# Kernel tuning notes

Hardware: AMD Instinct MI355X
Metric: run time of the kernel (lower is better)

The kernel has to match this reference:

```python
import math
import jax, jax.numpy as jnp
import numpy as np

B, H, W, C = 16, 64, 64, 192
WS, SHIFT, NH = 16, 8, 6
D = C // NH
N = WS * WS
HID = 4 * C
EPS = 1e-5


def _static_tables():
    # relative position index (N, N)
    coords = np.stack(np.meshgrid(np.arange(WS), np.arange(WS), indexing='ij'))  # (2, WS, WS)
    cf = coords.reshape(2, -1)
    rel = (cf[:, :, None] - cf[:, None, :]).transpose(1, 2, 0)  # (N, N, 2)
    rel[:, :, 0] += WS - 1
    rel[:, :, 1] += WS - 1
    rel[:, :, 0] *= 2 * WS - 1
    rel_idx = rel.sum(-1)  # (N, N)
    # log-spaced continuous relative coords table ((2WS-1)^2, 2)
    r = np.arange(-(WS - 1), WS, dtype=np.float32)
    tab = np.stack(np.meshgrid(r, r, indexing='ij'), axis=-1)  # (2WS-1, 2WS-1, 2)
    tab = tab / (WS - 1) * 8.0
    tab = np.sign(tab) * np.log2(np.abs(tab) + 1.0) / np.log2(8.0)
    # shifted-window attention mask (nW, N, N)
    img = np.zeros((H, W))
    cnt = 0
    for hs in (slice(0, -WS), slice(-WS, -SHIFT), slice(-SHIFT, None)):
        for ws_ in (slice(0, -WS), slice(-WS, -SHIFT), slice(-SHIFT, None)):
            img[hs, ws_] = cnt
            cnt += 1
    win = img.reshape(H // WS, WS, W // WS, WS).transpose(0, 2, 1, 3).reshape(-1, N)
    diff = win[:, None, :] - win[:, :, None]
    mask = np.where(diff != 0, -100.0, 0.0).astype(np.float32)
    return jnp.asarray(rel_idx), jnp.asarray(tab.reshape(-1, 2)), jnp.asarray(mask)

REL_IDX, CPB_TABLE, ATTN_MASK = _static_tables()


def setup_inputs() -> dict:
    key = jax.random.key(0)
    ks = jax.random.split(key, 24)
    s = 0.02
    return {
        'hidden_states': jax.random.normal(ks[0], (B, H * W, C), jnp.float32),
        'time': jax.random.uniform(ks[1], (B,), jnp.float32),
        'q_w': jax.random.normal(ks[2], (C, C), jnp.float32) * s,
        'q_b': jnp.zeros((C,), jnp.float32),
        'k_w': jax.random.normal(ks[3], (C, C), jnp.float32) * s,
        'v_w': jax.random.normal(ks[4], (C, C), jnp.float32) * s,
        'v_b': jnp.zeros((C,), jnp.float32),
        'logit_scale': jnp.full((NH, 1, 1), math.log(10.0), jnp.float32),
        'cpb_w1': jax.random.normal(ks[5], (512, 2), jnp.float32) * s,
        'cpb_b1': jnp.zeros((512,), jnp.float32),
        'cpb_w2': jax.random.normal(ks[6], (NH, 512), jnp.float32) * s,
        'proj_w': jax.random.normal(ks[7], (C, C), jnp.float32) * s,
        'proj_b': jnp.zeros((C,), jnp.float32),
        'ln1_ww': jax.random.normal(ks[8], (C, 1), jnp.float32) * s,
        'ln1_wb': jnp.ones((C,), jnp.float32),
        'ln1_bw': jax.random.normal(ks[9], (C, 1), jnp.float32) * s,
        'ln1_bb': jnp.zeros((C,), jnp.float32),
        'fc1_w': jax.random.normal(ks[10], (HID, C), jnp.float32) * s,
        'fc1_b': jnp.zeros((HID,), jnp.float32),
        'fc2_w': jax.random.normal(ks[11], (C, HID), jnp.float32) * s,
        'fc2_b': jnp.zeros((C,), jnp.float32),
        'ln2_ww': jax.random.normal(ks[12], (C, 1), jnp.float32) * s,
        'ln2_wb': jnp.ones((C,), jnp.float32),
        'ln2_bw': jax.random.normal(ks[13], (C, 1), jnp.float32) * s,
        'ln2_bb': jnp.zeros((C,), jnp.float32),
    }


def _cond_ln(x, time, ww, wb, bw, bb):
    mean = x.mean(-1, keepdims=True)
    var = (x ** 2).mean(-1, keepdims=True) - mean ** 2
    xn = (x - mean) / jnp.sqrt(var + EPS)
    t = time.reshape(-1, 1)
    w = (t @ ww.T + wb)[:, None, :]
    b = (t @ bw.T + bb)[:, None, :]
    return w * xn + b


def _forward(hidden_states, time, q_w, q_b, k_w, v_w, v_b, logit_scale,
             cpb_w1, cpb_b1, cpb_w2, proj_w, proj_b,
             ln1_ww, ln1_wb, ln1_bw, ln1_bb,
             fc1_w, fc1_b, fc2_w, fc2_b,
             ln2_ww, ln2_wb, ln2_bw, ln2_bb):
    nWh, nWw = H // WS, W // WS
    nW = nWh * nWw
    x = hidden_states.reshape(B, H, W, C)
    x = jnp.roll(x, (-SHIFT, -SHIFT), axis=(1, 2))
    # window partition -> (B*nW, N, C)
    xw = x.reshape(B, nWh, WS, nWw, WS, C).transpose(0, 1, 3, 2, 4, 5).reshape(-1, N, C)
    q = (xw @ q_w.T + q_b).reshape(-1, N, NH, D).transpose(0, 2, 1, 3)
    k = (xw @ k_w.T).reshape(-1, N, NH, D).transpose(0, 2, 1, 3)
    v = (xw @ v_w.T + v_b).reshape(-1, N, NH, D).transpose(0, 2, 1, 3)
    # cosine attention with learned temperature
    qn = q / jnp.linalg.norm(q, axis=-1, keepdims=True)
    kn = k / jnp.linalg.norm(k, axis=-1, keepdims=True)
    scale = jnp.exp(jnp.minimum(logit_scale, math.log(100.0)))  # (NH,1,1)
    attn = jnp.einsum('whnd,whmd->whnm', qn, kn) * scale
    # continuous relative position bias
    tbl = jnp.maximum(CPB_TABLE @ cpb_w1.T + cpb_b1, 0.0) @ cpb_w2.T  # (M, NH)
    rpb = tbl[REL_IDX.reshape(-1)].reshape(N, N, NH).transpose(2, 0, 1)
    attn = attn + 16.0 * jax.nn.sigmoid(rpb)[None]
    # shifted-window mask
    attn = attn.reshape(B, nW, NH, N, N) + ATTN_MASK[None, :, None]
    attn = jax.nn.softmax(attn.reshape(-1, NH, N, N), axis=-1)
    out = jnp.einsum('whnm,whmd->whnd', attn, v).transpose(0, 2, 1, 3).reshape(-1, N, C)
    out = out @ proj_w.T + proj_b
    # window reverse + un-roll
    out = out.reshape(B, nWh, nWw, WS, WS, C).transpose(0, 1, 3, 2, 4, 5).reshape(B, H, W, C)
    out = jnp.roll(out, (SHIFT, SHIFT), axis=(1, 2)).reshape(B, H * W, C)
    # res-post-norm residual blocks
    h = hidden_states + _cond_ln(out, time, ln1_ww, ln1_wb, ln1_bw, ln1_bb)
    mlp = jax.nn.gelu(h @ fc1_w.T + fc1_b, approximate=False) @ fc2_w.T + fc2_b
    return h + _cond_ln(mlp, time, ln2_ww, ln2_wb, ln2_bw, ln2_bb)


def reference(hidden_states, time, q_w, q_b, k_w, v_w, v_b, logit_scale,
              cpb_w1, cpb_b1, cpb_w2, proj_w, proj_b,
              ln1_ww, ln1_wb, ln1_bw, ln1_bb,
              fc1_w, fc1_b, fc2_w, fc2_b,
              ln2_ww, ln2_wb, ln2_bw, ln2_bb):
    return _forward(hidden_states, time, q_w, q_b, k_w, v_w, v_b, logit_scale,
                    cpb_w1, cpb_b1, cpb_w2, proj_w, proj_b,
                    ln1_ww, ln1_wb, ln1_bw, ln1_bb,
                    fc1_w, fc1_b, fc2_w, fc2_b,
                    ln2_ww, ln2_wb, ln2_bw, ln2_bb)
```

## Files before the change

kernel.cpp:

```cpp
#include <hip/hip_runtime.h>
#include <hip/hip_bf16.h>
#include <hip/hip_fp16.h>
#include <math.h>

#define BB 16
#define CC 192
#define SHIFT 8
#define NH 6
#define DD 32
#define NN 256
#define HID 768
#define NWIN 256
#define NROWS 65536

#define OFF_TBL   0ll
#define OFF_BIASM (32ll<<10)
#define OFF_WQKV  (3200ll<<10)
#define OFF_PWB   (3424ll<<10)
#define OFF_W1B   (3500ll<<10)
#define OFF_W2B   (3800ll<<10)
#define OFF_BQKV  (4096ll<<10)
#define OFF_WTAB  (4104ll<<10)
#define OFF_XB    (8ll<<20)
#define OFF_Q     (32ll<<20)
#define OFF_K     (56ll<<20)
#define OFF_V     (80ll<<20)
#define OFF_AO    (104ll<<20)
#define OFF_HB    OFF_XB
#define OFF_H2    OFF_Q

typedef __attribute__((ext_vector_type(4)))  float f32x4;
typedef __attribute__((ext_vector_type(16))) float f32x16;
typedef __attribute__((ext_vector_type(8)))  short bf16x8;

__device__ __forceinline__ void gload16(const void* g, void* l) {
    __builtin_amdgcn_global_load_lds(
        (const __attribute__((address_space(1))) void*)g,
        (__attribute__((address_space(3))) void*)l, 16, 0, 0);
}

__device__ __forceinline__ float b2f(short s) {
    unsigned u = ((unsigned)(unsigned short)s) << 16;
    return __builtin_bit_cast(float, u);
}
__device__ __forceinline__ short f2b(float f) {
    return __builtin_bit_cast(short, __float2bfloat16(f));
}
__device__ __forceinline__ unsigned pk2(float lo, float hi) {
    unsigned a = (unsigned short)f2b(lo);
    unsigned b = (unsigned short)f2b(hi);
    return a | (b << 16);
}

__device__ __forceinline__ float fexp2(float x) {
#if __has_builtin(__builtin_amdgcn_exp2f)
    return __builtin_amdgcn_exp2f(x);
#else
    return __expf(x * 0.69314718056f);
#endif
}

__device__ __forceinline__ float gelu_fast(float x) {
    float x2 = x * x;
    float z = x * fmaf(0.0713548353f, x2, 1.5957691216f);
    float e = __expf(-z);
    return x * __builtin_amdgcn_rcpf(1.0f + e);
}

__device__ __forceinline__ float cpb_coord(int u) {
    float t = (float)u * (8.0f / 15.0f);
    return copysignf(log2f(fabsf(t) + 1.0f) * (1.0f / 3.0f), t);
}

__global__ __launch_bounds__(512) void k_tbl(
    const float* __restrict__ w1, const float* __restrict__ b1,
    const float* __restrict__ w2, float* __restrict__ tbl)
{
    __shared__ float r[512];
    int m = blockIdx.x;
    int a = m / 31, b = m % 31;
    float c0 = cpb_coord(a - 15);
    float c1 = cpb_coord(b - 15);
    int hd = threadIdx.x;
    float rv = c0 * w1[hd * 2 + 0] + c1 * w1[hd * 2 + 1] + b1[hd];
    r[hd] = fmaxf(rv, 0.0f);
    __syncthreads();
    if (hd < NH) {
        float s = 0.0f;
        for (int k = 0; k < 512; ++k) s += r[k] * w2[hd * 512 + k];
        tbl[m * NH + hd] = s;
    }
}

__global__ __launch_bounds__(256) void k_biasm(
    const float* __restrict__ tbl, const float* __restrict__ lscale,
    __half* __restrict__ biasp)
{
    int bid = blockIdx.x;
    int ty = bid / (NH * NN);
    int rem = bid % (NH * NN);
    int h = rem >> 8, i = rem & 255;
    int j = threadIdx.x;
    int yi = i >> 4, xi = i & 15, yj = j >> 4, xj = j & 15;
    int idx = (yi - yj + 15) * 31 + (xi - xj + 15);
    float v = 16.0f / (1.0f + __expf(-tbl[idx * NH + h]));
    int rhi = (ty & 2) ? ((yi < SHIFT) ? 1 : 2) : 0;
    int rwi = (ty & 1) ? ((xi < SHIFT) ? 1 : 2) : 0;
    int rhj = (ty & 2) ? ((yj < SHIFT) ? 1 : 2) : 0;
    int rwj = (ty & 1) ? ((xj < SHIFT) ? 1 : 2) : 0;
    if (rhi * 3 + rwi != rhj * 3 + rwj) v -= 100.0f;
    float scale = __expf(fminf(lscale[h], 4.6051702f));
    v = (v - 16.0f - scale) * 1.44269504f;
    int jc = j & 31;
    int r = (jc & 3) + 4 * (jc >> 3);
    int g = (jc >> 2) & 1;
    int pos = (j & ~31) + g * 16 + r;
    biasp[(((size_t)ty * NH + h) * NN + i) * NN + pos] = __float2half(v);
}

__global__ __launch_bounds__(256) void k_cvt(
    const float* __restrict__ qw, const float* __restrict__ kw,
    const float* __restrict__ vw, const float* __restrict__ pw,
    const float* __restrict__ fc1w, const float* __restrict__ fc2w,
    const float* __restrict__ q_b, const float* __restrict__ v_b,
    __hip_bfloat16* __restrict__ wqkv, __hip_bfloat16* __restrict__ pwb,
    __hip_bfloat16* __restrict__ w1b, __hip_bfloat16* __restrict__ w2b,
    float* __restrict__ bqkv)
{
    int i = blockIdx.x * 256 + threadIdx.x;
    const int S1 = 36864, S2 = 73728, S3 = 110592, S4 = 147456,
              S5 = 294912, S6 = 442368, S7 = 442944;
    if (i < S3) {
        const float* src = (i < S1) ? qw : (i < S2) ? kw : vw;
        int off = (i < S1) ? i : (i < S2) ? i - S1 : i - S2;
        wqkv[i] = __float2bfloat16(src[off]);
    } else if (i < S4) { pwb[i - S3] = __float2bfloat16(pw[i - S3]); }
    else if (i < S5)   { w1b[i - S4] = __float2bfloat16(fc1w[i - S4]); }
    else if (i < S6)   { w2b[i - S5] = __float2bfloat16(fc2w[i - S5]); }
    else if (i < S7) {
        int j = i - S6;
        bqkv[j] = (j < 192) ? q_b[j] : (j < 384) ? 0.0f : v_b[j - 384];
    }
}

__global__ __launch_bounds__(256) void k_wtab(
    const float* __restrict__ time,
    const float* __restrict__ w1w, const float* __restrict__ w1b_,
    const float* __restrict__ b1w, const float* __restrict__ b1b_,
    const float* __restrict__ w2w, const float* __restrict__ w2b_,
    const float* __restrict__ b2w, const float* __restrict__ b2b_,
    float* __restrict__ wtab)
{
    int idx = blockIdx.x * 256 + threadIdx.x;
    int t = idx / 3072, rem = idx % 3072;
    int b = rem / 192, c = rem % 192;
    float tm = time[b];
    float v;
    if (t == 0)      v = tm * w1w[c] + w1b_[c];
    else if (t == 1) v = tm * b1w[c] + b1b_[c];
    else if (t == 2) v = tm * w2w[c] + w2b_[c];
    else             v = tm * b2w[c] + b2b_[c];
    wtab[idx] = v;
}

__global__ __launch_bounds__(256) void k_gather(
    const float* __restrict__ x, __hip_bfloat16* __restrict__ xb)
{
    int idx = blockIdx.x * 256 + threadIdx.x;
    int r = idx / 48, c4 = idx % 48;
    int win = r >> 8, n = r & 255;
    int b = win >> 4, wh = (win >> 2) & 3, ww = win & 3;
    int yi = n >> 4, xi = n & 15;
    int sy = (wh * 16 + yi + SHIFT) & 63;
    int sx = (ww * 16 + xi + SHIFT) & 63;
    float4 v = *(const float4*)&x[((size_t)b * 4096 + sy * 64 + sx) * CC + c4 * 4];
    union { short h[4]; short4 s4; } u;
    u.h[0] = f2b(v.x); u.h[1] = f2b(v.y); u.h[2] = f2b(v.z); u.h[3] = f2b(v.w);
    *(short4*)&((short*)xb)[(size_t)r * CC + c4 * 4] = u.s4;
}

#define STAGE_SWZ(dstLds, srcPtr, ldK, nR)                                  \
    for (int r_ = 0; r_ < (nR); ++r_) {                                     \
        int off_ = r_ * 256 + tid;                                          \
        int row_ = off_ >> 3, cb_ = off_ & 7;                               \
        int ce_ = ((cb_ ^ (row_ & 7)) << 3);                                \
        gload16((srcPtr) + (size_t)row_ * (ldK) + ce_, &(dstLds)[off_ * 8]); \
    }

__global__ __launch_bounds__(256) void k_qkvgemm(
    const __hip_bfloat16* __restrict__ A, const __hip_bfloat16* __restrict__ Bw,
    const float* __restrict__ bias, const float* __restrict__ lscale,
    __hip_bfloat16* __restrict__ qbo, __hip_bfloat16* __restrict__ kbo,
    __hip_bfloat16* __restrict__ vbo)
{
    __shared__ short lds[12288];
    short* As = lds;
    short* Bs = lds + 8192;
    int tid = threadIdx.x, lane = tid & 63;
    int w = tid >> 6, wr = w >> 1, wc = w & 1;
    int bm = blockIdx.x, bn = blockIdx.y;

    f32x4 acc[4][2];
    #pragma unroll
    for (int fm = 0; fm < 4; ++fm)
        #pragma unroll
        for (int fn = 0; fn < 2; ++fn) acc[fm][fn] = (f32x4)0.0f;

    for (int kt = 0; kt < CC; kt += 64) {
        STAGE_SWZ(As, A + (size_t)(bm * 128) * CC + kt, CC, 4)
        STAGE_SWZ(Bs, Bw + (size_t)(bn * 64) * CC + kt, CC, 2)
        __syncthreads();
        #pragma unroll
        for (int kk = 0; kk < 2; ++kk) {
            int kcq = kk * 4 + (lane >> 4);
            bf16x8 af[4], bfr[2];
            #pragma unroll
            for (int fm = 0; fm < 4; ++fm) {
                int row = wr * 64 + fm * 16 + (lane & 15);
                af[fm] = *(const bf16x8*)&As[row * 64 + ((kcq ^ (row & 7)) << 3)];
            }
            #pragma unroll
            for (int fn = 0; fn < 2; ++fn) {
                int row = wc * 32 + fn * 16 + (lane & 15);
                bfr[fn] = *(const bf16x8*)&Bs[row * 64 + ((kcq ^ (row & 7)) << 3)];
            }
            #pragma unroll
            for (int fm = 0; fm < 4; ++fm)
                #pragma unroll
                for (int fn = 0; fn < 2; ++fn)
                    acc[fm][fn] = __builtin_amdgcn_mfma_f32_16x16x32_bf16(
                        af[fm], bfr[fn], acc[fm][fn], 0, 0, 0);
        }
        __syncthreads();
    }

    bool donorm = (bn < 6);
    bool isq = (bn < 3);
    float qscale = __expf(fminf(lscale[(bn % 3) * 2 + wc], 4.6051702f)) * 1.44269504f;
    int bcol = bn * 64 + wc * 32 + (lane & 15);
    #pragma unroll
    for (int fm = 0; fm < 4; ++fm)
        #pragma unroll
        for (int r = 0; r < 4; ++r) {
            float v0 = acc[fm][0][r] + bias[bcol];
            float v1 = acc[fm][1][r] + bias[bcol + 16];
            if (donorm) {
                float s2 = v0 * v0 + v1 * v1;
                s2 += __shfl_xor(s2, 1);
                s2 += __shfl_xor(s2, 2);
                s2 += __shfl_xor(s2, 4);
                s2 += __shfl_xor(s2, 8);
                float rn = rsqrtf(s2);
                if (isq) rn *= qscale;
                v0 *= rn; v1 *= rn;
            }
            int rowl = wr * 64 + fm * 16 + ((lane >> 4) << 2) + r;
            int c0 = wc * 32 + (lane & 15);
            int sw = (rowl & 3) << 4;
            lds[rowl * 64 + (c0 ^ sw)] = f2b(v0);
            lds[rowl * 64 + ((c0 + 16) ^ sw)] = f2b(v1);
        }
    __syncthreads();
    __hip_bfloat16* dst = (bn < 3) ? qbo : (bn < 6) ? kbo : vbo;
    int cb0 = (bn % 3) * 64;
    #pragma unroll
    for (int rr = 0; rr < 2; ++rr) {
        int row = rr * 64 + (tid >> 2);
        int cl = (tid & 3) * 16;
        int cp = cl ^ ((row & 3) << 4);
        bf16x8 a = *(const bf16x8*)&lds[row * 64 + cp];
        bf16x8 b = *(const bf16x8*)&lds[row * 64 + cp + 8];
        size_t base = (size_t)(bm * 128 + row) * CC + cb0 + cl;
        *(bf16x8*)&dst[base] = a;
        *(bf16x8*)&dst[base + 8] = b;
    }
}

#define VTP 260
__global__ __launch_bounds__(256, 3) void k_attn(
    const __hip_bfloat16* __restrict__ qb,
    const __hip_bfloat16* __restrict__ kb,
    const __hip_bfloat16* __restrict__ vb,
    const __half* __restrict__ biasp,
    __hip_bfloat16* __restrict__ ao)
{
    __shared__ short Vt[32 * VTP];
    int blk = blockIdx.x;
    int win = blk / NH, h = blk % NH;
    int wwh = (win >> 2) & 3, www = win & 3;
    int ty = (((wwh == 3) ? 2 : 0) | ((www == 3) ? 1 : 0));
    int tid = threadIdx.x;
    int wv = tid >> 6, lane = tid & 63;
    int c = lane & 31, g = lane >> 5;

    {
        int j = wv * 64 + lane;
        const short* vsrc = (const short*)vb + ((size_t)(win * NN + j)) * CC + h * DD;
        #pragma unroll
        for (int q4 = 0; q4 < 4; ++q4) {
            bf16x8 t = *(const bf16x8*)(vsrc + q4 * 8);
            #pragma unroll
            for (int e = 0; e < 8; ++e)
                Vt[(q4 * 8 + e) * VTP + j] = t[e];
        }
    }
    __syncthreads();

    const short* qsrc = (const short*)qb + ((size_t)(win * NN + wv * 64)) * CC + h * DD;
    bf16x8 qf[2][2];
    #pragma unroll
    for (int fq = 0; fq < 2; ++fq)
        #pragma unroll
        for (int kd = 0; kd < 2; ++kd)
            qf[fq][kd] = *(const bf16x8*)(qsrc + (size_t)(32 * fq + c) * CC + 16 * kd + 8 * g);

    f32x16 acc_o[2];
    acc_o[0] = (f32x16)0.0f; acc_o[1] = (f32x16)0.0f;
    float lsum[2] = {0.0f, 0.0f};

    const short* kbase = (const short*)kb + ((size_t)(win * NN)) * CC + h * DD;
    const __half* bbase = biasp + (((size_t)ty * NH + h) * NN) * NN;

    for (int t = 0; t < 4; ++t) {
        int jt = t * 64;
        #pragma unroll
        for (int fj = 0; fj < 2; ++fj) {
            int jb = jt + 32 * fj;
            bf16x8 kf0 = *(const bf16x8*)(kbase + (size_t)(jb + c) * CC + 8 * g);
            bf16x8 kf1 = *(const bf16x8*)(kbase + (size_t)(jb + c) * CC + 16 + 8 * g);
            f32x16 st[2];
            __builtin_amdgcn_s_setprio(1);
            {
                f32x16 t0 = __builtin_amdgcn_mfma_f32_32x32x16_bf16(
                    kf0, qf[0][0], (f32x16)0.0f, 0, 0, 0);
                st[0] = __builtin_amdgcn_mfma_f32_32x32x16_bf16(
                    kf1, qf[0][1], t0, 0, 0, 0);
                f32x16 t1 = __builtin_amdgcn_mfma_f32_32x32x16_bf16(
                    kf0, qf[1][0], (f32x16)0.0f, 0, 0, 0);
                st[1] = __builtin_amdgcn_mfma_f32_32x32x16_bf16(
                    kf1, qf[1][1], t1, 0, 0, 0);
            }
            __builtin_amdgcn_s_setprio(0);
            bf16x8 vfr[2];
            #pragma unroll
            for (int rb = 0; rb < 2; ++rb) {
                int j0 = jb + 16 * rb + 4 * g;
                uint2 va = *(const uint2*)&Vt[c * VTP + j0];
                uint2 vb2 = *(const uint2*)&Vt[c * VTP + j0 + 8];
                union { unsigned u[4]; bf16x8 v; } vu;
                vu.u[0] = va.x; vu.u[1] = va.y; vu.u[2] = vb2.x; vu.u[3] = vb2.y;
                vfr[rb] = vu.v;
            }
            #pragma unroll
            for (int fq = 0; fq < 2; ++fq) {
                const __half* bp = bbase + (size_t)(wv * 64 + 32 * fq + c) * NN
                                   + jb + g * 16;
                union { uint4 u; __half2 h2[4]; } ba, bbu;
                ba.u  = *(const uint4*)bp;
                bbu.u = *(const uint4*)(bp + 8);
                float p[16];
                #pragma unroll
                for (int q4 = 0; q4 < 4; ++q4) {
                    float2 fa = __half22float2(ba.h2[q4]);
                    p[2 * q4 + 0] = st[fq][2 * q4 + 0] + fa.x;
                    p[2 * q4 + 1] = st[fq][2 * q4 + 1] + fa.y;
                    float2 fb = __half22float2(bbu.h2[q4]);
                    p[8 + 2 * q4 + 0] = st[fq][8 + 2 * q4 + 0] + fb.x;
                    p[8 + 2 * q4 + 1] = st[fq][8 + 2 * q4 + 1] + fb.y;
                }
                #pragma unroll
                for (int r = 0; r < 16; ++r) p[r] = fexp2(p[r]);
                #pragma unroll
                for (int r = 0; r < 16; ++r) lsum[fq] += p[r];
                union { unsigned u[4]; bf16x8 v; } pu0, pu1;
                pu0.u[0] = pk2(p[0],  p[1]);  pu0.u[1] = pk2(p[2],  p[3]);
                pu0.u[2] = pk2(p[4],  p[5]);  pu0.u[3] = pk2(p[6],  p[7]);
                pu1.u[0] = pk2(p[8],  p[9]);  pu1.u[1] = pk2(p[10], p[11]);
                pu1.u[2] = pk2(p[12], p[13]); pu1.u[3] = pk2(p[14], p[15]);
                __builtin_amdgcn_s_setprio(1);
                acc_o[fq] = __builtin_amdgcn_mfma_f32_32x32x16_bf16(
                    pu0.v, vfr[0], acc_o[fq], 0, 0, 0);
                acc_o[fq] = __builtin_amdgcn_mfma_f32_32x32x16_bf16(
                    pu1.v, vfr[1], acc_o[fq], 0, 0, 0);
                __builtin_amdgcn_s_setprio(0);
            }
        }
    }

    #pragma unroll
    for (int fq = 0; fq < 2; ++fq) {
        lsum[fq] += __shfl_xor(lsum[fq], 32);
        float rlv = 1.0f / lsum[fq];
        #pragma unroll
        for (int r = 0; r < 16; ++r) {
            int rho = (r & 3) + 8 * (r >> 2) + 4 * g;
            float rli = __shfl(rlv, rho);
            int row = wv * 64 + 32 * fq + rho;
            ao[((size_t)(win * NN + row)) * CC + h * DD + c] =
                __float2bfloat16(acc_o[fq][r] * rli);
        }
    }
}

__global__ __launch_bounds__(256) void k_projgemm(
    const __hip_bfloat16* __restrict__ ao,
    const __hip_bfloat16* __restrict__ pwb,
    const float* __restrict__ pbias,
    const float* __restrict__ wtab,
    __hip_bfloat16* xbhb)
{
    __shared__ short lds[16384];
    __shared__ float part[64][4];
    short* As = lds;
    short* Bs = lds + 4096;
    int tid = threadIdx.x, lane = tid & 63;
    int w = tid >> 6, wr = w >> 1, wc = w & 1;
    int bm = blockIdx.x;

    f32x4 acc[2][6];
    #pragma unroll
    for (int fm = 0; fm < 2; ++fm)
        #pragma unroll
        for (int fn = 0; fn < 6; ++fn) acc[fm][fn] = (f32x4)0.0f;

    for (int kt = 0; kt < CC; kt += 64) {
        STAGE_SWZ(As, ao + (size_t)(bm * 64) * CC + kt, CC, 2)
        STAGE_SWZ(Bs, pwb + kt, CC, 6)
        __syncthreads();
        #pragma unroll
        for (int kk = 0; kk < 2; ++kk) {
            int kcq = kk * 4 + (lane >> 4);
            bf16x8 af[2], bfr[6];
            #pragma unroll
            for (int fm = 0; fm < 2; ++fm) {
                int row = wr * 32 + fm * 16 + (lane & 15);
                af[fm] = *(const bf16x8*)&As[row * 64 + ((kcq ^ (row & 7)) << 3)];
            }
            #pragma unroll
            for (int fn = 0; fn < 6; ++fn) {
                int row = wc * 96 + fn * 16 + (lane & 15);
                bfr[fn] = *(const bf16x8*)&Bs[row * 64 + ((kcq ^ (row & 7)) << 3)];
            }
            #pragma unroll
            for (int fm = 0; fm < 2; ++fm)
                #pragma unroll
                for (int fn = 0; fn < 6; ++fn)
                    acc[fm][fn] = __builtin_amdgcn_mfma_f32_16x16x32_bf16(
                        af[fm], bfr[fn], acc[fm][fn], 0, 0, 0);
        }
        __syncthreads();
    }

    #pragma unroll
    for (int fm = 0; fm < 2; ++fm)
        #pragma unroll
        for (int r = 0; r < 4; ++r) {
            int rowl = wr * 32 + fm * 16 + ((lane >> 4) << 2) + r;
            float s = 0.0f, s2 = 0.0f;
            #pragma unroll
            for (int fn = 0; fn < 6; ++fn) {
                int col = wc * 96 + fn * 16 + (lane & 15);
                float v = acc[fm][fn][r] + pbias[col];
                lds[rowl * 200 + col] = f2b(v);
                s += v; s2 += v * v;
            }
            #pragma unroll
            for (int m = 1; m < 16; m <<= 1) {
                s  += __shfl_xor(s, m);
                s2 += __shfl_xor(s2, m);
            }
            if ((lane & 15) == 0) {
                part[rowl][wc * 2]     = s;
                part[rowl][wc * 2 + 1] = s2;
            }
        }
    __syncthreads();

    int row = tid >> 2;
    int cb = (tid & 3) * 48;
    float s  = part[row][0] + part[row][2];
    float s2 = part[row][1] + part[row][3];
    float mean = s * (1.0f / 192.0f);
    float rstd = rsqrtf(s2 * (1.0f / 192.0f) - mean * mean + 1e-5f);
    int rw = bm * 64 + row;
    const float* wt = wtab + (rw >> 12) * 192;
    const float* bt = wtab + 16 * 192 + (rw >> 12) * 192;
    #pragma unroll
    for (int c8 = 0; c8 < 6; ++c8) {
        int c = cb + c8 * 8;
        bf16x8 lv = *(const bf16x8*)&lds[row * 200 + c];
        bf16x8 xv = *(const bf16x8*)&xbhb[(size_t)rw * CC + c];
        float4 w0 = *(const float4*)&wt[c], w1 = *(const float4*)&wt[c + 4];
        float4 b0 = *(const float4*)&bt[c], b1 = *(const float4*)&bt[c + 4];
        float wv[8] = {w0.x, w0.y, w0.z, w0.w, w1.x, w1.y, w1.z, w1.w};
        float bv[8] = {b0.x, b0.y, b0.z, b0.w, b1.x, b1.y, b1.z, b1.w};
        bf16x8 o;
        #pragma unroll
        for (int e = 0; e < 8; ++e) {
            float xn = (b2f(lv[e]) - mean) * rstd;
            o[e] = f2b(b2f(xv[e]) + wv[e] * xn + bv[e]);
        }
        *(bf16x8*)&xbhb[(size_t)rw * CC + c] = o;
    }
}

__global__ __launch_bounds__(256) void k_fc1(
    const __hip_bfloat16* __restrict__ A, const __hip_bfloat16* __restrict__ Bw,
    const float* __restrict__ bias, __hip_bfloat16* __restrict__ Cout)
{
    __shared__ short lds[16384];
    short* As = lds;
    short* Bs = lds + 8192;
    int tid = threadIdx.x;
    int lane = tid & 63;
    int w = tid >> 6, wr = w >> 1, wc = w & 1;
    int bm = blockIdx.x, bn = blockIdx.y;

    f32x4 acc[4][4];
    #pragma unroll
    for (int fm = 0; fm < 4; ++fm)
        #pragma unroll
        for (int fn = 0; fn < 4; ++fn)
            acc[fm][fn] = (f32x4)0.0f;

    for (int kt = 0; kt < CC; kt += 64) {
        STAGE_SWZ(As, A + (size_t)(bm * 128) * CC + kt, CC, 4)
        STAGE_SWZ(Bs, Bw + (size_t)(bn * 128) * CC + kt, CC, 4)
        __syncthreads();
        #pragma unroll
        for (int kk = 0; kk < 2; ++kk) {
            int kcq = kk * 4 + (lane >> 4);
            bf16x8 af[4], bfr[4];
            #pragma unroll
            for (int fm = 0; fm < 4; ++fm) {
                int row = wr * 64 + fm * 16 + (lane & 15);
                af[fm] = *(const bf16x8*)&As[row * 64 + ((kcq ^ (row & 7)) << 3)];
            }
            #pragma unroll
            for (int fn = 0; fn < 4; ++fn) {
                int row = wc * 64 + fn * 16 + (lane & 15);
                bfr[fn] = *(const bf16x8*)&Bs[row * 64 + ((kcq ^ (row & 7)) << 3)];
            }
            #pragma unroll
            for (int fm = 0; fm < 4; ++fm)
                #pragma unroll
                for (int fn = 0; fn < 4; ++fn)
                    acc[fm][fn] = __builtin_amdgcn_mfma_f32_16x16x32_bf16(
                        af[fm], bfr[fn], acc[fm][fn], 0, 0, 0);
        }
        __syncthreads();
    }

    #pragma unroll
    for (int fm = 0; fm < 4; ++fm)
        #pragma unroll
        for (int fn = 0; fn < 4; ++fn) {
            int coll = wc * 64 + fn * 16 + (lane & 15);
            float bv = bias[bn * 128 + coll];
            #pragma unroll
            for (int r = 0; r < 4; ++r) {
                int rowl = wr * 64 + fm * 16 + ((lane >> 4) << 2) + r;
                float v = gelu_fast(acc[fm][fn][r] + bv);
                lds[rowl * 128 + (coll ^ ((rowl & 7) << 4))] = f2b(v);
            }
        }
    __syncthreads();
    #pragma unroll
    for (int rr = 0; rr < 4; ++rr) {
        int row = rr * 32 + (tid >> 3);
        int cl = (tid & 7) * 16;
        int cp = cl ^ ((row & 7) << 4);
        bf16x8 a = *(const bf16x8*)&lds[row * 128 + cp];
        bf16x8 b = *(const bf16x8*)&lds[row * 128 + cp + 8];
        size_t base = (size_t)(bm * 128 + row) * HID + bn * 128 + cl;
        *(bf16x8*)&Cout[base] = a;
        *(bf16x8*)&Cout[base + 8] = b;
    }
}

__global__ __launch_bounds__(256) void k_fc2ln(
    const __hip_bfloat16* __restrict__ A,
    const __hip_bfloat16* __restrict__ Bw,
    const float* __restrict__ bias,
    const __hip_bfloat16* __restrict__ hb,
    const float* __restrict__ wtab,
    float* __restrict__ out)
{
    __shared__ short lds[16384];
    __shared__ float part[64][4];
    short* As = lds;
    short* Bs = lds + 4096;
    int tid = threadIdx.x, lane = tid & 63;
    int w = tid >> 6, wr = w >> 1, wc = w & 1;
    int bm = blockIdx.x;

    f32x4 acc[2][6];
    #pragma unroll
    for (int fm = 0; fm < 2; ++fm)
        #pragma unroll
        for (int fn = 0; fn < 6; ++fn) acc[fm][fn] = (f32x4)0.0f;

    for (int kt = 0; kt < HID; kt += 64) {
        STAGE_SWZ(As, A + (size_t)(bm * 64) * HID + kt, HID, 2)
        STAGE_SWZ(Bs, Bw + kt, HID, 6)
        __syncthreads();
        #pragma unroll
        for (int kk = 0; kk < 2; ++kk) {
            int kcq = kk * 4 + (lane >> 4);
            bf16x8 af[2], bfr[6];
            #pragma unroll
            for (int fm = 0; fm < 2; ++fm) {
                int row = wr * 32 + fm * 16 + (lane & 15);
                af[fm] = *(const bf16x8*)&As[row * 64 + ((kcq ^ (row & 7)) << 3)];
            }
            #pragma unroll
            for (int fn = 0; fn < 6; ++fn) {
                int row = wc * 96 + fn * 16 + (lane & 15);
                bfr[fn] = *(const bf16x8*)&Bs[row * 64 + ((kcq ^ (row & 7)) << 3)];
            }
            #pragma unroll
            for (int fm = 0; fm < 2; ++fm)
                #pragma unroll
                for (int fn = 0; fn < 6; ++fn)
                    acc[fm][fn] = __builtin_amdgcn_mfma_f32_16x16x32_bf16(
                        af[fm], bfr[fn], acc[fm][fn], 0, 0, 0);
        }
        __syncthreads();
    }

    #pragma unroll
    for (int fm = 0; fm < 2; ++fm)
        #pragma unroll
        for (int r = 0; r < 4; ++r) {
            int rowl = wr * 32 + fm * 16 + ((lane >> 4) << 2) + r;
            float s = 0.0f, s2 = 0.0f;
            #pragma unroll
            for (int fn = 0; fn < 6; ++fn) {
                int col = wc * 96 + fn * 16 + (lane & 15);
                float v = acc[fm][fn][r] + bias[col];
                lds[rowl * 200 + col] = f2b(v);
                s += v; s2 += v * v;
            }
            #pragma unroll
            for (int m = 1; m < 16; m <<= 1) {
                s  += __shfl_xor(s, m);
                s2 += __shfl_xor(s2, m);
            }
            if ((lane & 15) == 0) {
                part[rowl][wc * 2]     = s;
                part[rowl][wc * 2 + 1] = s2;
            }
        }
    __syncthreads();

    int row = tid >> 2;
    int cb = (tid & 3) * 48;
    float s  = part[row][0] + part[row][2];
    float s2 = part[row][1] + part[row][3];
    float mean = s * (1.0f / 192.0f);
    float rstd = rsqrtf(s2 * (1.0f / 192.0f) - mean * mean + 1e-5f);
    int rw = bm * 64 + row;
    int win = rw >> 8, n = rw & 255, b = rw >> 12;
    int wh = (win >> 2) & 3, wwn = win & 3;
    int y  = (wh * 16 + (n >> 4) + SHIFT) & 63;
    int xq = (wwn * 16 + (n & 15) + SHIFT) & 63;
    size_t rimg = (size_t)b * 4096 + y * 64 + xq;
    const float* wt = wtab + 2 * 16 * 192 + b * 192;
    const float* bt = wtab + 3 * 16 * 192 + b * 192;
    #pragma unroll
    for (int c8 = 0; c8 < 6; ++c8) {
        int c = cb + c8 * 8;
        bf16x8 lv = *(const bf16x8*)&lds[row * 200 + c];
        bf16x8 hv = *(const bf16x8*)&hb[(size_t)rw * CC + c];
        float4 w0 = *(const float4*)&wt[c], w1 = *(const float4*)&wt[c + 4];
        float4 b0 = *(const float4*)&bt[c], b1 = *(const float4*)&bt[c + 4];
        float wv[8] = {w0.x, w0.y, w0.z, w0.w, w1.x, w1.y, w1.z, w1.w};
        float bv[8] = {b0.x, b0.y, b0.z, b0.w, b1.x, b1.y, b1.z, b1.w};
        float4 o0, o1;
        float oo[8];
        #pragma unroll
        for (int e = 0; e < 8; ++e) {
            float xn = (b2f(lv[e]) - mean) * rstd;
            oo[e] = b2f(hv[e]) + wv[e] * xn + bv[e];
        }
        o0.x = oo[0]; o0.y = oo[1]; o0.z = oo[2]; o0.w = oo[3];
        o1.x = oo[4]; o1.y = oo[5]; o1.z = oo[6]; o1.w = oo[7];
        *(float4*)&out[rimg * CC + c] = o0;
        *(float4*)&out[rimg * CC + c + 4] = o1;
    }
}

extern "C" void kernel_launch(void* const* d_in, const int* in_sizes, int n_in,
                              void* d_out, int out_size, void* d_ws, size_t ws_size,
                              hipStream_t stream)
{
    const float* x        = (const float*)d_in[0];
    const float* time     = (const float*)d_in[1];
    const float* q_w      = (const float*)d_in[2];
    const float* q_b      = (const float*)d_in[3];
    const float* k_w      = (const float*)d_in[4];
    const float* v_w      = (const float*)d_in[5];
    const float* v_b      = (const float*)d_in[6];
    const float* lscale   = (const float*)d_in[7];
    const float* cpb_w1   = (const float*)d_in[8];
    const float* cpb_b1   = (const float*)d_in[9];
    const float* cpb_w2   = (const float*)d_in[10];
    const float* proj_w   = (const float*)d_in[11];
    const float* proj_b   = (const float*)d_in[12];
    const float* ln1_ww   = (const float*)d_in[13];
    const float* ln1_wb   = (const float*)d_in[14];
    const float* ln1_bw   = (const float*)d_in[15];
    const float* ln1_bb   = (const float*)d_in[16];
    const float* fc1_w    = (const float*)d_in[17];
    const float* fc1_b    = (const float*)d_in[18];
    const float* fc2_w    = (const float*)d_in[19];
    const float* fc2_b    = (const float*)d_in[20];
    const float* ln2_ww   = (const float*)d_in[21];
    const float* ln2_wb   = (const float*)d_in[22];
    const float* ln2_bw   = (const float*)d_in[23];
    const float* ln2_bb   = (const float*)d_in[24];

    char* ws = (char*)d_ws;
    float* tbl            = (float*)(ws + OFF_TBL);
    __half* biasp         = (__half*)(ws + OFF_BIASM);
    __hip_bfloat16* wqkv  = (__hip_bfloat16*)(ws + OFF_WQKV);
    __hip_bfloat16* pwb   = (__hip_bfloat16*)(ws + OFF_PWB);
    __hip_bfloat16* w1b   = (__hip_bfloat16*)(ws + OFF_W1B);
    __hip_bfloat16* w2b   = (__hip_bfloat16*)(ws + OFF_W2B);
    float* bqkv           = (float*)(ws + OFF_BQKV);
    float* wtab           = (float*)(ws + OFF_WTAB);
    __hip_bfloat16* xb    = (__hip_bfloat16*)(ws + OFF_XB);
    __hip_bfloat16* qb    = (__hip_bfloat16*)(ws + OFF_Q);
    __hip_bfloat16* kb    = (__hip_bfloat16*)(ws + OFF_K);
    __hip_bfloat16* vb    = (__hip_bfloat16*)(ws + OFF_V);
    __hip_bfloat16* ao    = (__hip_bfloat16*)(ws + OFF_AO);
    __hip_bfloat16* hb    = (__hip_bfloat16*)(ws + OFF_HB);
    __hip_bfloat16* h2    = (__hip_bfloat16*)(ws + OFF_H2);
    float* out            = (float*)d_out;

    k_tbl   <<<961, 512, 0, stream>>>(cpb_w1, cpb_b1, cpb_w2, tbl);
    k_biasm <<<4 * NH * NN, 256, 0, stream>>>(tbl, lscale, biasp);
    k_cvt   <<<1731, 256, 0, stream>>>(q_w, k_w, v_w, proj_w, fc1_w, fc2_w,
                                       q_b, v_b, wqkv, pwb, w1b, w2b, bqkv);
    k_wtab  <<<48, 256, 0, stream>>>(time, ln1_ww, ln1_wb, ln1_bw, ln1_bb,
                                     ln2_ww, ln2_wb, ln2_bw, ln2_bb, wtab);
    k_gather<<<12288, 256, 0, stream>>>(x, xb);
    k_qkvgemm<<<dim3(NROWS / 128, 9), 256, 0, stream>>>(xb, wqkv, bqkv, lscale, qb, kb, vb);
    k_attn  <<<NWIN * NH, 256, 0, stream>>>(qb, kb, vb, biasp, ao);
    k_projgemm<<<NROWS / 64, 256, 0, stream>>>(ao, pwb, proj_b, wtab, xb);
    k_fc1   <<<dim3(NROWS / 128, HID / 128), 256, 0, stream>>>(hb, w1b, fc1_b, h2);
    k_fc2ln <<<NROWS / 64, 256, 0, stream>>>(h2, w2b, fc2_b, hb, wtab, out);
}
```

Measured before the change: 249.6 us.

## Fuse fc1, GELU and fc2+LayerNorm into one MLP kernel; enlarge proj tile

Merges the fc1 GEMM, GELU and the fc2 GEMM with its conditional LayerNorm into a single kernel. Each 64-row block keeps its input rows in LDS and streams 64-wide hidden chunks through LDS, so the 65536x768 hidden activation is never written to or read from global memory. The residual input is also read back from LDS instead of global. Separately, the projection GEMM tile grows from 64 to 128 rows. The cost is more LDS per block, fewer blocks for the projection, and extra synchronisation inside the hidden-chunk loop.

```diff
diff --git a/kernel.cpp b/kernel.cpp
--- a/kernel.cpp
+++ b/kernel.cpp
@@ -27,7 +27,6 @@
 #define OFF_V     (80ll<<20)
 #define OFF_AO    (104ll<<20)
 #define OFF_HB    OFF_XB
-#define OFF_H2    OFF_Q
 
 typedef __attribute__((ext_vector_type(4)))  float f32x4;
 typedef __attribute__((ext_vector_type(16))) float f32x16;
@@ -409,31 +408,31 @@
     const float* __restrict__ wtab,
     __hip_bfloat16* xbhb)
 {
-    __shared__ short lds[16384];
-    __shared__ float part[64][4];
+    __shared__ short lds[25600];
+    __shared__ float part[128][4];
     short* As = lds;
-    short* Bs = lds + 4096;
+    short* Bs = lds + 8192;
     int tid = threadIdx.x, lane = tid & 63;
     int w = tid >> 6, wr = w >> 1, wc = w & 1;
     int bm = blockIdx.x;
 
-    f32x4 acc[2][6];
-    #pragma unroll
-    for (int fm = 0; fm < 2; ++fm)
+    f32x4 acc[4][6];
+    #pragma unroll
+    for (int fm = 0; fm < 4; ++fm)
         #pragma unroll
         for (int fn = 0; fn < 6; ++fn) acc[fm][fn] = (f32x4)0.0f;
 
     for (int kt = 0; kt < CC; kt += 64) {
-        STAGE_SWZ(As, ao + (size_t)(bm * 64) * CC + kt, CC, 2)
+        STAGE_SWZ(As, ao + (size_t)(bm * 128) * CC + kt, CC, 4)
         STAGE_SWZ(Bs, pwb + kt, CC, 6)
         __syncthreads();
         #pragma unroll
         for (int kk = 0; kk < 2; ++kk) {
             int kcq = kk * 4 + (lane >> 4);
-            bf16x8 af[2], bfr[6];
-            #pragma unroll
-            for (int fm = 0; fm < 2; ++fm) {
-                int row = wr * 32 + fm * 16 + (lane & 15);
+            bf16x8 af[4], bfr[6];
+            #pragma unroll
+            for (int fm = 0; fm < 4; ++fm) {
+                int row = wr * 64 + fm * 16 + (lane & 15);
                 af[fm] = *(const bf16x8*)&As[row * 64 + ((kcq ^ (row & 7)) << 3)];
             }
             #pragma unroll
@@ -442,7 +441,7 @@
                 bfr[fn] = *(const bf16x8*)&Bs[row * 64 + ((kcq ^ (row & 7)) << 3)];
             }
             #pragma unroll
-            for (int fm = 0; fm < 2; ++fm)
+            for (int fm = 0; fm < 4; ++fm)
                 #pragma unroll
                 for (int fn = 0; fn < 6; ++fn)
                     acc[fm][fn] = __builtin_amdgcn_mfma_f32_16x16x32_bf16(
@@ -452,10 +451,10 @@
     }
 
     #pragma unroll
-    for (int fm = 0; fm < 2; ++fm)
+    for (int fm = 0; fm < 4; ++fm)
         #pragma unroll
         for (int r = 0; r < 4; ++r) {
-            int rowl = wr * 32 + fm * 16 + ((lane >> 4) << 2) + r;
+            int rowl = wr * 64 + fm * 16 + ((lane >> 4) << 2) + r;
             float s = 0.0f, s2 = 0.0f;
             #pragma unroll
             for (int fn = 0; fn < 6; ++fn) {
@@ -476,17 +475,17 @@
         }
     __syncthreads();
 
-    int row = tid >> 2;
-    int cb = (tid & 3) * 48;
+    int row = tid >> 1;
+    int cb = (tid & 1) * 96;
     float s  = part[row][0] + part[row][2];
     float s2 = part[row][1] + part[row][3];
     float mean = s * (1.0f / 192.0f);
     float rstd = rsqrtf(s2 * (1.0f / 192.0f) - mean * mean + 1e-5f);
-    int rw = bm * 64 + row;
+    int rw = bm * 128 + row;
     const float* wt = wtab + (rw >> 12) * 192;
     const float* bt = wtab + 16 * 192 + (rw >> 12) * 192;
     #pragma unroll
-    for (int c8 = 0; c8 < 6; ++c8) {
+    for (int c8 = 0; c8 < 12; ++c8) {
         int c = cb + c8 * 8;
         bf16x8 lv = *(const bf16x8*)&lds[row * 200 + c];
         bf16x8 xv = *(const bf16x8*)&xbhb[(size_t)rw * CC + c];
@@ -504,106 +503,89 @@
     }
 }
 
-__global__ __launch_bounds__(256) void k_fc1(
-    const __hip_bfloat16* __restrict__ A, const __hip_bfloat16* __restrict__ Bw,
-    const float* __restrict__ bias, __hip_bfloat16* __restrict__ Cout)
-{
-    __shared__ short lds[16384];
-    short* As = lds;
-    short* Bs = lds + 8192;
-    int tid = threadIdx.x;
-    int lane = tid & 63;
-    int w = tid >> 6, wr = w >> 1, wc = w & 1;
-    int bm = blockIdx.x, bn = blockIdx.y;
-
-    f32x4 acc[4][4];
-    #pragma unroll
-    for (int fm = 0; fm < 4; ++fm)
-        #pragma unroll
-        for (int fn = 0; fn < 4; ++fn)
-            acc[fm][fn] = (f32x4)0.0f;
-
-    for (int kt = 0; kt < CC; kt += 64) {
-        STAGE_SWZ(As, A + (size_t)(bm * 128) * CC + kt, CC, 4)
-        STAGE_SWZ(Bs, Bw + (size_t)(bn * 128) * CC + kt, CC, 4)
-        __syncthreads();
-        #pragma unroll
-        for (int kk = 0; kk < 2; ++kk) {
-            int kcq = kk * 4 + (lane >> 4);
-            bf16x8 af[4], bfr[4];
-            #pragma unroll
-            for (int fm = 0; fm < 4; ++fm) {
-                int row = wr * 64 + fm * 16 + (lane & 15);
-                af[fm] = *(const bf16x8*)&As[row * 64 + ((kcq ^ (row & 7)) << 3)];
-            }
-            #pragma unroll
-            for (int fn = 0; fn < 4; ++fn) {
-                int row = wc * 64 + fn * 16 + (lane & 15);
-                bfr[fn] = *(const bf16x8*)&Bs[row * 64 + ((kcq ^ (row & 7)) << 3)];
-            }
-            #pragma unroll
-            for (int fm = 0; fm < 4; ++fm)
-                #pragma unroll
-                for (int fn = 0; fn < 4; ++fn)
-                    acc[fm][fn] = __builtin_amdgcn_mfma_f32_16x16x32_bf16(
-                        af[fm], bfr[fn], acc[fm][fn], 0, 0, 0);
-        }
-        __syncthreads();
-    }
-
-    #pragma unroll
-    for (int fm = 0; fm < 4; ++fm)
-        #pragma unroll
-        for (int fn = 0; fn < 4; ++fn) {
-            int coll = wc * 64 + fn * 16 + (lane & 15);
-            float bv = bias[bn * 128 + coll];
-            #pragma unroll
-            for (int r = 0; r < 4; ++r) {
-                int rowl = wr * 64 + fm * 16 + ((lane >> 4) << 2) + r;
-                float v = gelu_fast(acc[fm][fn][r] + bv);
-                lds[rowl * 128 + (coll ^ ((rowl & 7) << 4))] = f2b(v);
-            }
-        }
-    __syncthreads();
-    #pragma unroll
-    for (int rr = 0; rr < 4; ++rr) {
-        int row = rr * 32 + (tid >> 3);
-        int cl = (tid & 7) * 16;
-        int cp = cl ^ ((row & 7) << 4);
-        bf16x8 a = *(const bf16x8*)&lds[row * 128 + cp];
-        bf16x8 b = *(const bf16x8*)&lds[row * 128 + cp + 8];
-        size_t base = (size_t)(bm * 128 + row) * HID + bn * 128 + cl;
-        *(bf16x8*)&Cout[base] = a;
-        *(bf16x8*)&Cout[base + 8] = b;
-    }
-}
-
-__global__ __launch_bounds__(256) void k_fc2ln(
-    const __hip_bfloat16* __restrict__ A,
-    const __hip_bfloat16* __restrict__ Bw,
-    const float* __restrict__ bias,
+__global__ __launch_bounds__(256, 2) void k_mlp(
     const __hip_bfloat16* __restrict__ hb,
+    const __hip_bfloat16* __restrict__ w1b,
+    const float* __restrict__ b1,
+    const __hip_bfloat16* __restrict__ w2b,
+    const float* __restrict__ b2,
     const float* __restrict__ wtab,
     float* __restrict__ out)
 {
-    __shared__ short lds[16384];
-    __shared__ float part[64][4];
-    short* As = lds;
-    short* Bs = lds + 4096;
+    __shared__ short lds[40960];
+    short* As  = lds;
+    short* W1c = lds + 12288;
+    short* H2c = lds + 24576;
+    short* W2c = lds + 28672;
+    short* VAL = lds + 12288;
+    float* part = (float*)&lds[28672];
+
     int tid = threadIdx.x, lane = tid & 63;
     int w = tid >> 6, wr = w >> 1, wc = w & 1;
     int bm = blockIdx.x;
-
-    f32x4 acc[2][6];
+    size_t rb = (size_t)bm * 64;
+
+    #pragma unroll
+    for (int kt = 0; kt < 3; ++kt)
+        STAGE_SWZ(As + kt * 4096, hb + rb * CC + kt * 64, CC, 2)
+
+    f32x4 acc2[2][6];
     #pragma unroll
     for (int fm = 0; fm < 2; ++fm)
         #pragma unroll
-        for (int fn = 0; fn < 6; ++fn) acc[fm][fn] = (f32x4)0.0f;
-
-    for (int kt = 0; kt < HID; kt += 64) {
-        STAGE_SWZ(As, A + (size_t)(bm * 64) * HID + kt, HID, 2)
-        STAGE_SWZ(Bs, Bw + kt, HID, 6)
+        for (int fn = 0; fn < 6; ++fn) acc2[fm][fn] = (f32x4)0.0f;
+
+    for (int it = 0; it < 12; ++it) {
         __syncthreads();
+        #pragma unroll
+        for (int kt = 0; kt < 3; ++kt)
+            STAGE_SWZ(W1c + kt * 4096, w1b + (size_t)(it * 64) * CC + kt * 64, CC, 2)
+        STAGE_SWZ(W2c, w2b + it * 64, HID, 6)
+        __syncthreads();
+
+        f32x4 acc1[2][2];
+        #pragma unroll
+        for (int fm = 0; fm < 2; ++fm)
+            #pragma unroll
+            for (int fn = 0; fn < 2; ++fn) acc1[fm][fn] = (f32x4)0.0f;
+        #pragma unroll
+        for (int kt = 0; kt < 3; ++kt)
+            #pragma unroll
+            for (int kk = 0; kk < 2; ++kk) {
+                int kcq = kk * 4 + (lane >> 4);
+                bf16x8 af[2], bfr[2];
+                #pragma unroll
+                for (int fm = 0; fm < 2; ++fm) {
+                    int row = wr * 32 + fm * 16 + (lane & 15);
+                    af[fm] = *(const bf16x8*)&As[kt * 4096 + row * 64 + ((kcq ^ (row & 7)) << 3)];
+                }
+                #pragma unroll
+                for (int fn = 0; fn < 2; ++fn) {
+                    int row = wc * 32 + fn * 16 + (lane & 15);
+                    bfr[fn] = *(const bf16x8*)&W1c[kt * 4096 + row * 64 + ((kcq ^ (row & 7)) << 3)];
+                }
+                #pragma unroll
+                for (int fm = 0; fm < 2; ++fm)
+                    #pragma unroll
+                    for (int fn = 0; fn < 2; ++fn)
+                        acc1[fm][fn] = __builtin_amdgcn_mfma_f32_16x16x32_bf16(
+                            af[fm], bfr[fn], acc1[fm][fn], 0, 0, 0);
+            }
+        #pragma unroll
+        for (int fm = 0; fm < 2; ++fm)
+            #pragma unroll
+            for (int fn = 0; fn < 2; ++fn) {
+                int coll = wc * 32 + fn * 16 + (lane & 15);
+                float bv = b1[it * 64 + coll];
+                #pragma unroll
+                for (int r = 0; r < 4; ++r) {
+                    int rowl = wr * 32 + fm * 16 + ((lane >> 4) << 2) + r;
+                    float v = gelu_fast(acc1[fm][fn][r] + bv);
+                    H2c[rowl * 64 + (((coll >> 3) ^ (rowl & 7)) << 3) + (coll & 7)] = f2b(v);
+                }
+            }
+        __syncthreads();
+
         #pragma unroll
         for (int kk = 0; kk < 2; ++kk) {
             int kcq = kk * 4 + (lane >> 4);
@@ -611,22 +593,22 @@
             #pragma unroll
             for (int fm = 0; fm < 2; ++fm) {
                 int row = wr * 32 + fm * 16 + (lane & 15);
-                af[fm] = *(const bf16x8*)&As[row * 64 + ((kcq ^ (row & 7)) << 3)];
+                af[fm] = *(const bf16x8*)&H2c[row * 64 + ((kcq ^ (row & 7)) << 3)];
             }
             #pragma unroll
             for (int fn = 0; fn < 6; ++fn) {
                 int row = wc * 96 + fn * 16 + (lane & 15);
-                bfr[fn] = *(const bf16x8*)&Bs[row * 64 + ((kcq ^ (row & 7)) << 3)];
+                bfr[fn] = *(const bf16x8*)&W2c[row * 64 + ((kcq ^ (row & 7)) << 3)];
             }
             #pragma unroll
             for (int fm = 0; fm < 2; ++fm)
                 #pragma unroll
                 for (int fn = 0; fn < 6; ++fn)
-                    acc[fm][fn] = __builtin_amdgcn_mfma_f32_16x16x32_bf16(
-                        af[fm], bfr[fn], acc[fm][fn], 0, 0, 0);
-        }
-        __syncthreads();
-    }
+                    acc2[fm][fn] = __builtin_amdgcn_mfma_f32_16x16x32_bf16(
+                        af[fm], bfr[fn], acc2[fm][fn], 0, 0, 0);
+        }
+    }
+    __syncthreads();
 
     #pragma unroll
     for (int fm = 0; fm < 2; ++fm)
@@ -637,8 +619,8 @@
             #pragma unroll
             for (int fn = 0; fn < 6; ++fn) {
                 int col = wc * 96 + fn * 16 + (lane & 15);
-                float v = acc[fm][fn][r] + bias[col];
-                lds[rowl * 200 + col] = f2b(v);
+                float v = acc2[fm][fn][r] + b2[col];
+                VAL[rowl * 200 + col] = f2b(v);
                 s += v; s2 += v * v;
             }
             #pragma unroll
@@ -647,19 +629,19 @@
                 s2 += __shfl_xor(s2, m);
             }
             if ((lane & 15) == 0) {
-                part[rowl][wc * 2]     = s;
-                part[rowl][wc * 2 + 1] = s2;
+                part[rowl * 4 + wc * 2]     = s;
+                part[rowl * 4 + wc * 2 + 1] = s2;
             }
         }
     __syncthreads();
 
     int row = tid >> 2;
     int cb = (tid & 3) * 48;
-    float s  = part[row][0] + part[row][2];
-    float s2 = part[row][1] + part[row][3];
+    float s  = part[row * 4 + 0] + part[row * 4 + 2];
+    float s2 = part[row * 4 + 1] + part[row * 4 + 3];
     float mean = s * (1.0f / 192.0f);
     float rstd = rsqrtf(s2 * (1.0f / 192.0f) - mean * mean + 1e-5f);
-    int rw = bm * 64 + row;
+    int rw = (int)rb + row;
     int win = rw >> 8, n = rw & 255, b = rw >> 12;
     int wh = (win >> 2) & 3, wwn = win & 3;
     int y  = (wh * 16 + (n >> 4) + SHIFT) & 63;
@@ -670,8 +652,9 @@
     #pragma unroll
     for (int c8 = 0; c8 < 6; ++c8) {
         int c = cb + c8 * 8;
-        bf16x8 lv = *(const bf16x8*)&lds[row * 200 + c];
-        bf16x8 hv = *(const bf16x8*)&hb[(size_t)rw * CC + c];
+        bf16x8 lv = *(const bf16x8*)&VAL[row * 200 + c];
+        bf16x8 hv = *(const bf16x8*)&As[(c >> 6) * 4096 + row * 64 +
+                                        ((((c & 63) >> 3) ^ (row & 7)) << 3)];
         float4 w0 = *(const float4*)&wt[c], w1 = *(const float4*)&wt[c + 4];
         float4 b0 = *(const float4*)&bt[c], b1 = *(const float4*)&bt[c + 4];
         float wv[8] = {w0.x, w0.y, w0.z, w0.w, w1.x, w1.y, w1.z, w1.w};
@@ -735,7 +718,6 @@
     __hip_bfloat16* vb    = (__hip_bfloat16*)(ws + OFF_V);
     __hip_bfloat16* ao    = (__hip_bfloat16*)(ws + OFF_AO);
     __hip_bfloat16* hb    = (__hip_bfloat16*)(ws + OFF_HB);
-    __hip_bfloat16* h2    = (__hip_bfloat16*)(ws + OFF_H2);
     float* out            = (float*)d_out;
 
     k_tbl   <<<961, 512, 0, stream>>>(cpb_w1, cpb_b1, cpb_w2, tbl);
@@ -747,7 +729,6 @@
     k_gather<<<12288, 256, 0, stream>>>(x, xb);
     k_qkvgemm<<<dim3(NROWS / 128, 9), 256, 0, stream>>>(xb, wqkv, bqkv, lscale, qb, kb, vb);
     k_attn  <<<NWIN * NH, 256, 0, stream>>>(qb, kb, vb, biasp, ao);
-    k_projgemm<<<NROWS / 64, 256, 0, stream>>>(ao, pwb, proj_b, wtab, xb);
-    k_fc1   <<<dim3(NROWS / 128, HID / 128), 256, 0, stream>>>(hb, w1b, fc1_b, h2);
-    k_fc2ln <<<NROWS / 64, 256, 0, stream>>>(h2, w2b, fc2_b, hb, wtab, out);
-}
+    k_projgemm<<<NROWS / 128, 256, 0, stream>>>(ao, pwb, proj_b, wtab, xb);
+    k_mlp   <<<NROWS / 64, 256, 0, stream>>>(hb, w1b, fc1_b, w2b, fc2_b, wtab, out);
+}
```

New measurement: 230.4 us, median of 3. 7.7% less time.
